# Kernel tuning notes

Hardware: AMD Instinct MI355X
Metric: run time of the kernel (lower is better)

The kernel has to match this reference:

```python
import jax, jax.numpy as jnp
import numpy as np


def setup_inputs() -> dict:
    key = jax.random.key(0)
    k1, k2 = jax.random.split(key)
    B, T, C = 32, 512, 384
    MAX_LEN = 4096
    x = jax.random.normal(k1, (B, T, C), dtype=jnp.float32)
    duration = jax.random.randint(k2, (B, T), 0, 12, dtype=jnp.int64)
    return {"x": x, "duration": duration, "max_len": MAX_LEN}


def reference(x, duration, max_len):
    # x: [B, T, C] float; duration: [B, T] int; max_len: python int
    B, T, C = x.shape
    dur = jnp.maximum(duration, 0)            # original clamps expand_size at 0
    csum = jnp.cumsum(dur, axis=1)            # [B, T] exclusive boundaries (right edges)
    pos = jnp.arange(max_len)                 # [max_len]
    # source phoneme index for each output frame j: count of csum[b] <= j
    idx = jax.vmap(lambda c: jnp.searchsorted(c, pos, side="right"))(csum)  # [B, max_len]
    idx_c = jnp.clip(idx, 0, T - 1)
    out = jnp.take_along_axis(x, idx_c[:, :, None], axis=1)  # [B, max_len, C]
    mel_len = csum[:, -1]                     # [B] total expanded frames per batch
    valid = pos[None, :] < mel_len[:, None]   # [B, max_len], pad region -> 0
    out = out * valid[:, :, None].astype(out.dtype)
    return out, mel_len
```

## Files before the change

### kernel.cpp

```cpp
#include <hip/hip_runtime.h>
#include <hip/hip_bf16.h>


#define B   32
#define T   512
#define C   384
#define C4  96
#define ML  4096
#define PPB 128
#define TPB 256

typedef float v4f __attribute__((ext_vector_type(4)));

__global__ __launch_bounds__(TPB)
void lr_fused_kernel(const float* __restrict__ x,
                     const int* __restrict__ dur,
                     float* __restrict__ out,
                     float* __restrict__ mel_out) {
    __shared__ int s_cs[T];
    __shared__ int s_p[TPB];
    __shared__ int s_idx[PPB];

    const int tilesPerBatch = ML / PPB;
    const int b     = blockIdx.x / tilesPerBatch;
    const int ptile = blockIdx.x % tilesPerBatch;
    const int tid   = threadIdx.x;

    int2 d2 = ((const int2*)(dur + b * T))[tid];
    int d0 = d2.x < 0 ? 0 : d2.x;
    int d1 = d2.y < 0 ? 0 : d2.y;
    s_p[tid] = d0 + d1;
    __syncthreads();
    #pragma unroll
    for (int off = 1; off < TPB; off <<= 1) {
        int add = (tid >= off) ? s_p[tid - off] : 0;
        __syncthreads();
        s_p[tid] += add;
        __syncthreads();
    }
    const int S = s_p[tid];
    s_cs[2 * tid + 1] = S;
    s_cs[2 * tid]     = S - d1;
    __syncthreads();

    const int mel = s_cs[T - 1];
    if (ptile == 0 && tid == 0) mel_out[b] = (float)mel;

    if (tid < PPB) {
        const int p = ptile * PPB + tid;
        int r = -1;
        if (p < mel) {
            int lo = 0, hi = T;
            while (lo < hi) {
                int mid = (lo + hi) >> 1;
                if (s_cs[mid] <= p) lo = mid + 1; else hi = mid;
            }
            r = lo < (T - 1) ? lo : (T - 1);
        }
        s_idx[tid] = r;
    }
    __syncthreads();

    const v4f* __restrict__ x4 = (const v4f*)x;
    v4f* __restrict__ o4 = (v4f*)out;
    const size_t xbase = (size_t)b * T * C4;
    const size_t obase = (size_t)b * ML * C4 + (size_t)ptile * PPB * C4;
    const v4f zero = (v4f){0.f, 0.f, 0.f, 0.f};

    #pragma unroll 4
    for (int v = tid; v < PPB * C4; v += TPB) {
        const int pl = v / C4;
        const int c4 = v - pl * C4;
        const int t  = s_idx[pl];
        v4f val = zero;
        if (t >= 0) val = x4[xbase + (size_t)t * C4 + c4];
        __builtin_nontemporal_store(val, &o4[obase + v]);
    }
}

extern "C" void kernel_launch(void* const* d_in, const int* in_sizes, int n_in,
                              void* d_out, int out_size, void* d_ws, size_t ws_size,
                              hipStream_t stream) {
    const float* x   = (const float*)d_in[0];
    const int*   dur = (const int*)d_in[1];

    float* out     = (float*)d_out;
    float* mel_out = out + (size_t)B * ML * C;

    const int grid = B * (ML / PPB);
    lr_fused_kernel<<<grid, TPB, 0, stream>>>(x, dur, out, mel_out);
}
```

Baseline: 239.3 us.

## Use wavefront shuffle scan and 384-thread blocks with fixed per-thread channel mapping

```diff
diff --git a/kernel.cpp b/kernel.cpp
--- a/kernel.cpp
+++ b/kernel.cpp
@@ -4,11 +4,10 @@
 
 #define B   32
 #define T   512
-#define C   384
 #define C4  96
 #define ML  4096
 #define PPB 128
-#define TPB 256
+#define TPB 384
 
 typedef float v4f __attribute__((ext_vector_type(4)));
 
@@ -18,29 +17,38 @@
                      float* __restrict__ out,
                      float* __restrict__ mel_out) {
     __shared__ int s_cs[T];
-    __shared__ int s_p[TPB];
+    __shared__ int s_wsum[4];
     __shared__ int s_idx[PPB];
 
-    const int tilesPerBatch = ML / PPB;
-    const int b     = blockIdx.x / tilesPerBatch;
-    const int ptile = blockIdx.x % tilesPerBatch;
+    const int b     = blockIdx.x >> 5;
+    const int ptile = blockIdx.x & 31;
     const int tid   = threadIdx.x;
+    const int lane  = tid & 63;
 
-    int2 d2 = ((const int2*)(dur + b * T))[tid];
-    int d0 = d2.x < 0 ? 0 : d2.x;
-    int d1 = d2.y < 0 ? 0 : d2.y;
-    s_p[tid] = d0 + d1;
+    int pairsum = 0, d1 = 0;
+    if (tid < 256) {
+        int2 d2 = ((const int2*)(dur + b * T))[tid];
+        int d0 = d2.x < 0 ? 0 : d2.x;
+        d1     = d2.y < 0 ? 0 : d2.y;
+        pairsum = d0 + d1;
+    }
+    int incl = pairsum;
+    #pragma unroll
+    for (int off = 1; off < 64; off <<= 1) {
+        int n = __shfl_up(incl, off, 64);
+        if (lane >= off) incl += n;
+    }
+    if (tid < 256 && lane == 63) s_wsum[tid >> 6] = incl;
     __syncthreads();
-    #pragma unroll
-    for (int off = 1; off < TPB; off <<= 1) {
-        int add = (tid >= off) ? s_p[tid - off] : 0;
-        __syncthreads();
-        s_p[tid] += add;
-        __syncthreads();
+    if (tid < 256) {
+        const int w = tid >> 6;
+        int wp = 0;
+        #pragma unroll
+        for (int j = 0; j < 3; ++j) if (j < w) wp += s_wsum[j];
+        const int S = incl + wp;
+        s_cs[2 * tid + 1] = S;
+        s_cs[2 * tid]     = S - d1;
     }
-    const int S = s_p[tid];
-    s_cs[2 * tid + 1] = S;
-    s_cs[2 * tid]     = S - d1;
     __syncthreads();
 
     const int mel = s_cs[T - 1];
@@ -63,18 +71,19 @@
 
     const v4f* __restrict__ x4 = (const v4f*)x;
     v4f* __restrict__ o4 = (v4f*)out;
-    const size_t xbase = (size_t)b * T * C4;
-    const size_t obase = (size_t)b * ML * C4 + (size_t)ptile * PPB * C4;
+    const int sub = tid / 96;
+    const int c4  = tid - sub * 96;
+    const size_t xbase = (size_t)b * T * C4 + c4;
+    const size_t obase = (size_t)b * ML * C4 + (size_t)ptile * PPB * C4 + c4;
     const v4f zero = (v4f){0.f, 0.f, 0.f, 0.f};
 
-    #pragma unroll 4
-    for (int v = tid; v < PPB * C4; v += TPB) {
-        const int pl = v / C4;
-        const int c4 = v - pl * C4;
+    #pragma unroll 8
+    for (int k = 0; k < PPB / 4; ++k) {
+        const int pl = 4 * k + sub;
         const int t  = s_idx[pl];
         v4f val = zero;
-        if (t >= 0) val = x4[xbase + (size_t)t * C4 + c4];
-        __builtin_nontemporal_store(val, &o4[obase + v]);
+        if (t >= 0) val = x4[xbase + (size_t)t * C4];
+        o4[obase + (size_t)pl * C4] = val;
     }
 }
 
@@ -85,7 +94,7 @@
     const int*   dur = (const int*)d_in[1];
 
     float* out     = (float*)d_out;
-    float* mel_out = out + (size_t)B * ML * C;
+    float* mel_out = out + (size_t)B * ML * C4 * 4;
 
     const int grid = B * (ML / PPB);
     lr_fused_kernel<<<grid, TPB, 0, stream>>>(x, dur, out, mel_out);
```

After: 225.5 us. 1.06x faster.
